# Optimization experiments

Measured on AMD Instinct MI355X. Metric: run time of the kernel, lower is better.

The kernel has to match this reference:

```python
import jax, jax.numpy as jnp
import numpy as np

EPS = 1e-6
N_NODES = 50000
N_EDGES = 800000
IN_DIM = 128
OUT_DIM = 128
HEADS = 4
D_K = OUT_DIM // HEADS
ATT_DIM = 2 * D_K + 1  # use_edge_feat=True


def setup_inputs() -> dict:
    key = jax.random.key(0)
    ks = jax.random.split(key, 8)
    h = jax.random.normal(ks[0], (N_NODES, IN_DIM), dtype=jnp.float32)
    edge_index = jax.random.randint(ks[1], (2, N_EDGES), 0, N_NODES, dtype=jnp.int64)
    edge_feat = jax.random.normal(ks[2], (N_EDGES, 1), dtype=jnp.float32)
    # parameters
    W_w = jax.random.normal(ks[3], (OUT_DIM, IN_DIM), dtype=jnp.float32) / np.sqrt(IN_DIM)
    W_b = jnp.zeros((OUT_DIM,), dtype=jnp.float32)
    att = jax.random.normal(ks[4], (HEADS, ATT_DIM), dtype=jnp.float32)
    ln_g = jnp.ones((OUT_DIM,), dtype=jnp.float32)
    ln_b = jnp.zeros((OUT_DIM,), dtype=jnp.float32)
    return {"h": h, "edge_index": edge_index, "edge_feat": edge_feat,
            "W_w": W_w, "W_b": W_b, "att": att, "ln_g": ln_g, "ln_b": ln_b}


def _layer_norm(x, g, b):
    mu = jnp.mean(x, axis=-1, keepdims=True)
    var = jnp.mean(jnp.square(x - mu), axis=-1, keepdims=True)
    return (x - mu) * jax.lax.rsqrt(var + 1e-5) * g + b


def reference(h, edge_index, edge_feat, W_w, W_b, att, ln_g, ln_b):
    num_nodes = h.shape[0]
    z = h @ W_w.T + W_b                      # [N, out_dim]
    zr = z.reshape(num_nodes, HEADS, D_K)    # [N, H, d_k]
    src, dst = edge_index[0], edge_index[1]
    h_s = zr[src]                            # [E, H, d_k]
    h_d = zr[dst]                            # [E, H, d_k]
    f_e = jnp.broadcast_to(edge_feat[:, None, :], (edge_feat.shape[0], HEADS, 1))
    concat = jnp.concatenate([h_s, h_d, f_e], axis=-1)  # [E, H, att_dim]
    scores = jnp.sum(concat * att[None], axis=-1)        # [E, H]
    scores = jnp.where(scores >= 0, scores, 0.2 * scores)  # LeakyReLU(0.2)
    scores = jnp.clip(scores, -20.0, 20.0)
    alpha = jnp.exp(scores)                               # [E, H]
    denom = jax.ops.segment_sum(alpha, dst, num_segments=num_nodes)  # [N, H]
    norm_alpha = alpha / (denom[dst] + EPS)               # [E, H]
    weighted = h_s * norm_alpha[..., None]                # [E, H, d_k]
    out = jax.ops.segment_sum(weighted, dst, num_segments=num_nodes)  # [N, H, d_k]
    out = out.reshape(num_nodes, OUT_DIM) + z
    out = _layer_norm(out, ln_g, ln_b)
    return jax.nn.elu(out)
```

## Files before the change

### kernel.cpp

```cpp
#include <hip/hip_runtime.h>
#include <hip/hip_bf16.h>
#include <math.h>

typedef __attribute__((ext_vector_type(8))) short bf16x8;
typedef __attribute__((ext_vector_type(4))) float f32x4;

__device__ __forceinline__ unsigned short f2bf(float f) {
    unsigned u = __float_as_uint(f);
    unsigned r = ((u >> 16) & 1u) + 0x7fffu;
    return (unsigned short)((u + r) >> 16);
}
__device__ __forceinline__ float bfL(unsigned u) { return __uint_as_float(u << 16); }
__device__ __forceinline__ float bfH(unsigned u) { return __uint_as_float(u & 0xffff0000u); }

#define SCORE_NPB 128

__global__ __launch_bounds__(256) void k_prep(const float* __restrict__ W,
                                              const float* __restrict__ bias,
                                              const float* __restrict__ att,
                                              const float* __restrict__ h,
                                              unsigned short* __restrict__ Wb16,
                                              float* __restrict__ s_src,
                                              float* __restrict__ s_dst,
                                              int* __restrict__ head4,
                                              int N, int scoreBlocks) {
    const int t = threadIdx.x;
    const int bid = blockIdx.x;
    if (bid == 0) {
#pragma unroll
        for (int q = 0; q < 8; ++q) {
            int gi = q * 256 + t;
            int kg = gi >> 7, row = gi & 127;
            int kbase = (kg >> 2) * 32 + (kg & 3) * 4;
            unsigned pk[4];
#pragma unroll
            for (int p = 0; p < 4; ++p) {
                int e0 = 2 * p, e1 = 2 * p + 1;
                float v0 = W[(size_t)row * 128 + kbase + (e0 >> 2) * 16 + (e0 & 3)];
                float v1 = W[(size_t)row * 128 + kbase + (e1 >> 2) * 16 + (e1 & 3)];
                pk[p] = ((unsigned)f2bf(v1) << 16) | f2bf(v0);
            }
            *reinterpret_cast<uint4*>(&Wb16[(size_t)gi * 8]) =
                make_uint4(pk[0], pk[1], pk[2], pk[3]);
        }
    } else if (bid <= scoreBlocks) {
        __shared__ float wsdL[2][4][128];
        __shared__ float cs[8];
#pragma unroll
        for (int q = 0; q < 4; ++q) {
            int idx = q * 256 + t;
            int isD = idx >> 9, rem = idx & 511;
            int hd = rem >> 7, k = rem & 127;
            float w = 0.f;
            for (int j = 0; j < 32; ++j)
                w += W[(size_t)(hd * 32 + j) * 128 + k] * att[hd * 65 + isD * 32 + j];
            wsdL[isD][hd][k] = w;
        }
        if (t < 8) {
            int chd = t & 3, cIsD = t >> 2;
            float c = 0.f;
            for (int j = 0; j < 32; ++j)
                c += bias[chd * 32 + j] * att[chd * 65 + cIsD * 32 + j];
            cs[t] = c;
        }
        __syncthreads();
        const int p = t & 7;
#pragma unroll
        for (int it = 0; it < 4; ++it) {
            int node = (bid - 1) * SCORE_NPB + it * 32 + (t >> 3);
            if (node >= N) continue;
            const float* hp = h + (size_t)node * 128 + p * 16;
            float ss[4] = {0.f, 0.f, 0.f, 0.f}, sd[4] = {0.f, 0.f, 0.f, 0.f};
#pragma unroll
            for (int q = 0; q < 4; ++q) {
                float4 hv = *reinterpret_cast<const float4*>(hp + q * 4);
#pragma unroll
                for (int hd = 0; hd < 4; ++hd) {
                    const float* wa = &wsdL[0][hd][p * 16 + q * 4];
                    const float* wb = &wsdL[1][hd][p * 16 + q * 4];
                    ss[hd] += hv.x * wa[0] + hv.y * wa[1] + hv.z * wa[2] + hv.w * wa[3];
                    sd[hd] += hv.x * wb[0] + hv.y * wb[1] + hv.z * wb[2] + hv.w * wb[3];
                }
            }
#pragma unroll
            for (int off = 1; off < 8; off <<= 1)
#pragma unroll
                for (int hd = 0; hd < 4; ++hd) {
                    ss[hd] += __shfl_xor(ss[hd], off);
                    sd[hd] += __shfl_xor(sd[hd], off);
                }
            if (p == 0) {
                *reinterpret_cast<float4*>(&s_src[(size_t)node * 4]) =
                    make_float4(ss[0] + cs[0], ss[1] + cs[1], ss[2] + cs[2], ss[3] + cs[3]);
                *reinterpret_cast<float4*>(&s_dst[(size_t)node * 4]) =
                    make_float4(sd[0] + cs[4], sd[1] + cs[5], sd[2] + cs[6], sd[3] + cs[7]);
            }
        }
    } else {
        int i = ((bid - 1 - scoreBlocks) * 256 + t) * 4;
        if (i < N * 4)
            *reinterpret_cast<int4*>(&head4[i]) = make_int4(-1, -1, -1, -1);
    }
}

__global__ __launch_bounds__(256) void k_work(
        const float* __restrict__ h, const unsigned short* __restrict__ Wb16,
        const float* __restrict__ bias, unsigned short* __restrict__ zb16,
        const int* __restrict__ src, const int* __restrict__ dst,
        const float* __restrict__ ef, const float* __restrict__ att,
        const float* __restrict__ s_src, const float* __restrict__ s_dst,
        int* __restrict__ head4, int4* __restrict__ epkt,
        int N, int E, int gemmBlocks) {
    __shared__ short hS[16 * 64 * 8];
    const int t = threadIdx.x;
    const int bid = blockIdx.x;

    if (bid >= gemmBlocks) {
        int e = (bid - gemmBlocks) * 256 + t;
        if (e >= E) return;
        int s = src[e], d = dst[e];
        float fv = ef[e];
        int prev = atomicExch(&head4[(size_t)d * 4 + (e & 3)], e);
        float4 ss = *reinterpret_cast<const float4*>(&s_src[(size_t)s * 4]);
        float4 sd = *reinterpret_cast<const float4*>(&s_dst[(size_t)d * 4]);
        float aE0 = att[64], aE1 = att[129], aE2 = att[194], aE3 = att[259];
        float sc0 = ss.x + sd.x + fv * aE0;
        float sc1 = ss.y + sd.y + fv * aE1;
        float sc2 = ss.z + sd.z + fv * aE2;
        float sc3 = ss.w + sd.w + fv * aE3;
        sc0 = sc0 >= 0.f ? sc0 : 0.2f * sc0;  sc1 = sc1 >= 0.f ? sc1 : 0.2f * sc1;
        sc2 = sc2 >= 0.f ? sc2 : 0.2f * sc2;  sc3 = sc3 >= 0.f ? sc3 : 0.2f * sc3;
        float a0 = expf(fminf(fmaxf(sc0, -20.f), 20.f));
        float a1 = expf(fminf(fmaxf(sc1, -20.f), 20.f));
        float a2 = expf(fminf(fmaxf(sc2, -20.f), 20.f));
        float a3 = expf(fminf(fmaxf(sc3, -20.f), 20.f));
        epkt[e] = make_int4(s, prev,
            (int)(((unsigned)f2bf(a1) << 16) | f2bf(a0)),
            (int)(((unsigned)f2bf(a3) << 16) | f2bf(a2)));
        return;
    }

    const int by = bid & 1;
    const int n0 = (bid >> 1) * 64;
    const int obase = by * 64;
#pragma unroll
    for (int q = 0; q < 8; ++q) {
        int f = q * 256 + t;
        int nd = f >> 5;
        int k4 = (f & 31) * 4;
        int ks = k4 >> 5, rr = k4 & 31;
        int half = rr >> 4, g = (rr & 15) >> 2;
        int kg = ks * 4 + g;
        int slot = kg * 64 + (nd ^ (kg & 7));
        int hn = n0 + nd; if (hn > N - 1) hn = N - 1;
        float4 v = *reinterpret_cast<const float4*>(&h[(size_t)hn * 128 + k4]);
        uint2 pk = make_uint2(((unsigned)f2bf(v.y) << 16) | f2bf(v.x),
                              ((unsigned)f2bf(v.w) << 16) | f2bf(v.z));
        *reinterpret_cast<uint2*>(&hS[slot * 8 + half * 4]) = pk;
    }
    __syncthreads();

    const int wv = t >> 6, l = t & 63;
    const int la = l & 15, lb = l >> 4;
    const int nbase = wv * 16;
    const int node = n0 + nbase + la;

    bf16x8 hfr[4];
#pragma unroll
    for (int ks = 0; ks < 4; ++ks) {
        int kg = ks * 4 + lb;
        int slot = kg * 64 + ((nbase + la) ^ (kg & 7));
        hfr[ks] = *reinterpret_cast<const bf16x8*>(&hS[slot * 8]);
    }

#pragma unroll
    for (int ot = 0; ot < 4; ++ot) {
        f32x4 acc = {0.f, 0.f, 0.f, 0.f};
#pragma unroll
        for (int ks = 0; ks < 4; ++ks) {
            int kg = ks * 4 + lb;
            bf16x8 wfr = *reinterpret_cast<const bf16x8*>(
                &Wb16[((size_t)kg * 128 + obase + ot * 16 + la) * 8]);
            acc = __builtin_amdgcn_mfma_f32_16x16x32_bf16(wfr, hfr[ks], acc, 0, 0, 0);
        }
        int colb = obase + ot * 16 + lb * 4;
        float4 bq = *reinterpret_cast<const float4*>(&bias[colb]);
        if (node < N) {
            uint2 pk = make_uint2(
                ((unsigned)f2bf(acc[1] + bq.y) << 16) | f2bf(acc[0] + bq.x),
                ((unsigned)f2bf(acc[3] + bq.w) << 16) | f2bf(acc[2] + bq.z));
            *reinterpret_cast<uint2*>(&zb16[(size_t)node * 128 + colb]) = pk;
        }
    }
}

__global__ __launch_bounds__(128) void k_agg_final(const int* __restrict__ head4,
                                                   const int4* __restrict__ epkt,
                                                   const uint4* __restrict__ zb4,
                                                   const float* __restrict__ g,
                                                   const float* __restrict__ bparm,
                                                   float* __restrict__ out, int N) {
    int wave = threadIdx.x >> 6, lane = threadIdx.x & 63;
    int l8 = lane & 7;
    int n = blockIdx.x * 16 + wave * 8 + (lane >> 3);
    if (n >= N) return;
    const int hd = l8 >> 1;
    int4 eh = *reinterpret_cast<const int4*>(&head4[(size_t)n * 4]);
    int e0 = eh.x, e1 = eh.y, e2 = eh.z, e3 = eh.w;
    float X0 = 0.f, X1 = 0.f, X2 = 0.f, X3 = 0.f;
    float X4 = 0.f, X5 = 0.f, X6 = 0.f, X7 = 0.f;
    float X8 = 0.f, X9 = 0.f, Xa = 0.f, Xb = 0.f;
    float Xc = 0.f, Xd = 0.f, Xe = 0.f, Xf = 0.f;
    float da = 0.f;
#define UNPK(P, AV) { unsigned u = (hd & 2) ? (unsigned)(P).w : (unsigned)(P).z; \
    AV = (hd & 1) ? bfH(u) : bfL(u); }
#define STEP(EV) if (EV != -1) { \
        int4 p = epkt[EV]; \
        uint4 q0 = zb4[(size_t)p.x * 16 + l8 * 2]; \
        uint4 q1 = zb4[(size_t)p.x * 16 + l8 * 2 + 1]; \
        float a; UNPK(p, a) \
        X0 += bfL(q0.x) * a; X1 += bfH(q0.x) * a; \
        X2 += bfL(q0.y) * a; X3 += bfH(q0.y) * a; \
        X4 += bfL(q0.z) * a; X5 += bfH(q0.z) * a; \
        X6 += bfL(q0.w) * a; X7 += bfH(q0.w) * a; \
        X8 += bfL(q1.x) * a; X9 += bfH(q1.x) * a; \
        Xa += bfL(q1.y) * a; Xb += bfH(q1.y) * a; \
        Xc += bfL(q1.z) * a; Xd += bfH(q1.z) * a; \
        Xe += bfL(q1.w) * a; Xf += bfH(q1.w) * a; \
        da += a; EV = p.y; }
    while (((e0 & e1) & (e2 & e3)) != -1) {
        STEP(e0) STEP(e1) STEP(e2) STEP(e3)
    }
#undef STEP
#undef UNPK

    float inv = 1.f / (da + 1e-6f);
    uint4 qz0 = zb4[(size_t)n * 16 + l8 * 2];
    uint4 qz1 = zb4[(size_t)n * 16 + l8 * 2 + 1];
    float x0 = X0 * inv + bfL(qz0.x), x1 = X1 * inv + bfH(qz0.x);
    float x2 = X2 * inv + bfL(qz0.y), x3 = X3 * inv + bfH(qz0.y);
    float x4 = X4 * inv + bfL(qz0.z), x5 = X5 * inv + bfH(qz0.z);
    float x6 = X6 * inv + bfL(qz0.w), x7 = X7 * inv + bfH(qz0.w);
    float x8 = X8 * inv + bfL(qz1.x), x9 = X9 * inv + bfH(qz1.x);
    float xa = Xa * inv + bfL(qz1.y), xb = Xb * inv + bfH(qz1.y);
    float xc = Xc * inv + bfL(qz1.z), xd = Xd * inv + bfH(qz1.z);
    float xe = Xe * inv + bfL(qz1.w), xf = Xf * inv + bfH(qz1.w);
    float s = (((x0 + x1) + (x2 + x3)) + ((x4 + x5) + (x6 + x7)))
            + (((x8 + x9) + (xa + xb)) + ((xc + xd) + (xe + xf)));
#pragma unroll
    for (int off = 1; off < 8; off <<= 1) s += __shfl_xor(s, off);
    float mu = s * (1.f / 128.f);
    float d0 = x0 - mu, d1 = x1 - mu, d2 = x2 - mu, d3 = x3 - mu;
    float d4 = x4 - mu, d5 = x5 - mu, d6 = x6 - mu, d7 = x7 - mu;
    float d8 = x8 - mu, d9 = x9 - mu, dA = xa - mu, dB = xb - mu;
    float dC = xc - mu, dD = xd - mu, dE = xe - mu, dF = xf - mu;
    float q = (((d0 * d0 + d1 * d1) + (d2 * d2 + d3 * d3))
             + ((d4 * d4 + d5 * d5) + (d6 * d6 + d7 * d7)))
            + (((d8 * d8 + d9 * d9) + (dA * dA + dB * dB))
             + ((dC * dC + dD * dD) + (dE * dE + dF * dF)));
#pragma unroll
    for (int off = 1; off < 8; off <<= 1) q += __shfl_xor(q, off);
    float rstd = rsqrtf(q * (1.f / 128.f) + 1e-5f);
    const int c = l8 * 16;
    float dv[16] = {d0, d1, d2, d3, d4, d5, d6, d7, d8, d9, dA, dB, dC, dD, dE, dF};
#pragma unroll
    for (int qb = 0; qb < 4; ++qb) {
        float4 gg = *reinterpret_cast<const float4*>(&g[c + qb * 4]);
        float4 bb = *reinterpret_cast<const float4*>(&bparm[c + qb * 4]);
        float y0 = dv[qb * 4 + 0] * rstd * gg.x + bb.x;
        float y1 = dv[qb * 4 + 1] * rstd * gg.y + bb.y;
        float y2 = dv[qb * 4 + 2] * rstd * gg.z + bb.z;
        float y3 = dv[qb * 4 + 3] * rstd * gg.w + bb.w;
        y0 = y0 > 0.f ? y0 : expf(y0) - 1.f;
        y1 = y1 > 0.f ? y1 : expf(y1) - 1.f;
        y2 = y2 > 0.f ? y2 : expf(y2) - 1.f;
        y3 = y3 > 0.f ? y3 : expf(y3) - 1.f;
        *reinterpret_cast<float4*>(&out[(size_t)n * 128 + c + qb * 4]) =
            make_float4(y0, y1, y2, y3);
    }
}

extern "C" void kernel_launch(void* const* d_in, const int* in_sizes, int n_in,
                              void* d_out, int out_size, void* d_ws, size_t ws_size,
                              hipStream_t stream) {
    const float* h   = (const float*)d_in[0];
    const int*   ei  = (const int*)d_in[1];
    const float* ef  = (const float*)d_in[2];
    const float* Ww  = (const float*)d_in[3];
    const float* Wb  = (const float*)d_in[4];
    const float* att = (const float*)d_in[5];
    const float* lng = (const float*)d_in[6];
    const float* lnb = (const float*)d_in[7];
    float* out = (float*)d_out;

    const int N = in_sizes[0] / 128;
    const int E = in_sizes[1] / 2;
    const int* src = ei;
    const int* dst = ei + E;

    char* ws = (char*)d_ws;
    unsigned short* zb16   = (unsigned short*)ws; ws += (size_t)N * 128 * 2;
    unsigned short* Wb16   = (unsigned short*)ws; ws += (size_t)128 * 128 * 2;
    float*          s_src  = (float*)ws;          ws += (size_t)N * 4 * 4;
    float*          s_dst  = (float*)ws;          ws += (size_t)N * 4 * 4;
    int*            head4  = (int*)ws;            ws += (size_t)N * 4 * 4;
    int4*           epkt   = (int4*)ws;           ws += (size_t)E * 16;

    const int scoreBlocks = (N + SCORE_NPB - 1) / SCORE_NPB;
    const int headBlocks  = (N + 255) / 256;
    k_prep<<<1 + scoreBlocks + headBlocks, 256, 0, stream>>>(
        Ww, Wb, att, h, Wb16, s_src, s_dst, head4, N, scoreBlocks);

    const int gemmBlocks = ((N + 63) / 64) * 2;
    const int edgeBlocks = (E + 255) / 256;
    k_work<<<gemmBlocks + edgeBlocks, 256, 0, stream>>>(
        h, Wb16, Wb, zb16, src, dst, ef, att, s_src, s_dst, head4, epkt,
        N, E, gemmBlocks);
    k_agg_final<<<(N + 15) / 16, 128, 0, stream>>>(head4, epkt,
                                                   (const uint4*)zb16, lng, lnb, out, N);
}
```

Baseline: 110.2 us.

## Sort nodes by in-degree bins before aggregation to balance wave work

Counts the in-degree of every node with atomics, builds a 64-bin degree histogram, scans it and produces a node order grouped by degree. The aggregation kernel then processes nodes in that order, so the 8 nodes sharing a wave have similar edge-list lengths and lanes diverge less. It adds three small kernel launches, a counting pass of atomics over all edges, and an indirection through the order array, which scatters the output and z row accesses.

```diff
diff --git a/kernel.cpp b/kernel.cpp
--- a/kernel.cpp
+++ b/kernel.cpp
@@ -23,10 +23,13 @@
                                               float* __restrict__ s_src,
                                               float* __restrict__ s_dst,
                                               int* __restrict__ head4,
-                                              int N, int scoreBlocks) {
+                                              int* __restrict__ counts,
+                                              int* __restrict__ binCnt,
+                                              int N, int scoreBlocks, int headBlocks) {
     const int t = threadIdx.x;
     const int bid = blockIdx.x;
     if (bid == 0) {
+        if (t < 64) binCnt[t] = 0;
 #pragma unroll
         for (int q = 0; q < 8; ++q) {
             int gi = q * 256 + t;
@@ -96,10 +99,14 @@
                     make_float4(sd[0] + cs[4], sd[1] + cs[5], sd[2] + cs[6], sd[3] + cs[7]);
             }
         }
-    } else {
+    } else if (bid <= scoreBlocks + headBlocks) {
         int i = ((bid - 1 - scoreBlocks) * 256 + t) * 4;
         if (i < N * 4)
             *reinterpret_cast<int4*>(&head4[i]) = make_int4(-1, -1, -1, -1);
+    } else {
+        int i = ((bid - 1 - scoreBlocks - headBlocks) * 256 + t) * 4;
+        if (i < N)
+            *reinterpret_cast<int4*>(&counts[i]) = make_int4(0, 0, 0, 0);
     }
 }
 
@@ -110,11 +117,21 @@
         const float* __restrict__ ef, const float* __restrict__ att,
         const float* __restrict__ s_src, const float* __restrict__ s_dst,
         int* __restrict__ head4, int4* __restrict__ epkt,
-        int N, int E, int gemmBlocks) {
+        int* __restrict__ counts,
+        int N, int E, int gemmBlocks, int edgeBlocks) {
     __shared__ short hS[16 * 64 * 8];
     const int t = threadIdx.x;
     const int bid = blockIdx.x;
 
+    if (bid >= gemmBlocks + edgeBlocks) {
+        int base = (bid - gemmBlocks - edgeBlocks) * 1024 + t;
+#pragma unroll
+        for (int q = 0; q < 4; ++q) {
+            int e = base + q * 256;
+            if (e < E) atomicAdd(&counts[dst[e]], 1);
+        }
+        return;
+    }
     if (bid >= gemmBlocks) {
         int e = (bid - gemmBlocks) * 256 + t;
         if (e >= E) return;
@@ -194,7 +211,52 @@
     }
 }
 
-__global__ __launch_bounds__(128) void k_agg_final(const int* __restrict__ head4,
+__global__ __launch_bounds__(256) void k_binhist(const int* __restrict__ counts,
+                                                 int* __restrict__ binCnt, int N) {
+    __shared__ int lh[64];
+    int t = threadIdx.x;
+    if (t < 64) lh[t] = 0;
+    __syncthreads();
+    int i = blockIdx.x * 256 + t;
+    if (i < N) atomicAdd(&lh[min(counts[i], 63)], 1);
+    __syncthreads();
+    if (t < 64 && lh[t] > 0) atomicAdd(&binCnt[t], lh[t]);
+}
+
+__global__ void k_binscan(const int* __restrict__ binCnt,
+                          int* __restrict__ binCur) {
+    int lane = threadIdx.x & 63;
+    int x = binCnt[lane];
+    int own = x;
+#pragma unroll
+    for (int d = 1; d < 64; d <<= 1) {
+        int v = __shfl_up(x, d);
+        if (lane >= d) x += v;
+    }
+    binCur[lane] = x - own;
+}
+
+__global__ __launch_bounds__(256) void k_order(const int* __restrict__ counts,
+                                               int* __restrict__ binCur,
+                                               int* __restrict__ order, int N) {
+    __shared__ int lh[64], base[64];
+    int t = threadIdx.x;
+    if (t < 64) lh[t] = 0;
+    __syncthreads();
+    int i = blockIdx.x * 256 + t;
+    int b = 0, lrank = 0;
+    if (i < N) {
+        b = min(counts[i], 63);
+        lrank = atomicAdd(&lh[b], 1);
+    }
+    __syncthreads();
+    if (t < 64 && lh[t] > 0) base[t] = atomicAdd(&binCur[t], lh[t]);
+    __syncthreads();
+    if (i < N) order[base[b] + lrank] = i;
+}
+
+__global__ __launch_bounds__(128) void k_agg_final(const int* __restrict__ order,
+                                                   const int* __restrict__ head4,
                                                    const int4* __restrict__ epkt,
                                                    const uint4* __restrict__ zb4,
                                                    const float* __restrict__ g,
@@ -202,8 +264,9 @@
                                                    float* __restrict__ out, int N) {
     int wave = threadIdx.x >> 6, lane = threadIdx.x & 63;
     int l8 = lane & 7;
-    int n = blockIdx.x * 16 + wave * 8 + (lane >> 3);
-    if (n >= N) return;
+    int slot = blockIdx.x * 16 + wave * 8 + (lane >> 3);
+    if (slot >= N) return;
+    const int n = order[slot];
     const int hd = l8 >> 1;
     int4 eh = *reinterpret_cast<const int4*>(&head4[(size_t)n * 4]);
     int e0 = eh.x, e1 = eh.y, e2 = eh.z, e3 = eh.w;
@@ -304,18 +367,31 @@
     float*          s_src  = (float*)ws;          ws += (size_t)N * 4 * 4;
     float*          s_dst  = (float*)ws;          ws += (size_t)N * 4 * 4;
     int*            head4  = (int*)ws;            ws += (size_t)N * 4 * 4;
+    int*            counts = (int*)ws;            ws += (size_t)N * 4;
+    int*            order  = (int*)ws;            ws += (size_t)N * 4;
+    int*            binCnt = (int*)ws;            ws += (size_t)64 * 4;
+    int*            binCur = (int*)ws;            ws += (size_t)64 * 4;
     int4*           epkt   = (int4*)ws;           ws += (size_t)E * 16;
 
     const int scoreBlocks = (N + SCORE_NPB - 1) / SCORE_NPB;
     const int headBlocks  = (N + 255) / 256;
-    k_prep<<<1 + scoreBlocks + headBlocks, 256, 0, stream>>>(
-        Ww, Wb, att, h, Wb16, s_src, s_dst, head4, N, scoreBlocks);
+    const int cntBlocks   = (N / 4 + 255) / 256;
+    k_prep<<<1 + scoreBlocks + headBlocks + cntBlocks, 256, 0, stream>>>(
+        Ww, Wb, att, h, Wb16, s_src, s_dst, head4, counts, binCnt,
+        N, scoreBlocks, headBlocks);
 
     const int gemmBlocks = ((N + 63) / 64) * 2;
     const int edgeBlocks = (E + 255) / 256;
-    k_work<<<gemmBlocks + edgeBlocks, 256, 0, stream>>>(
-        h, Wb16, Wb, zb16, src, dst, ef, att, s_src, s_dst, head4, epkt,
-        N, E, gemmBlocks);
-    k_agg_final<<<(N + 15) / 16, 128, 0, stream>>>(head4, epkt,
+    const int histBlocks = (E + 1023) / 1024;
+    k_work<<<gemmBlocks + edgeBlocks + histBlocks, 256, 0, stream>>>(
+        h, Wb16, Wb, zb16, src, dst, ef, att, s_src, s_dst, head4, epkt, counts,
+        N, E, gemmBlocks, edgeBlocks);
+
+    const int nodeBlocks = (N + 255) / 256;
+    k_binhist<<<nodeBlocks, 256, 0, stream>>>(counts, binCnt, N);
+    k_binscan<<<1, 64, 0, stream>>>(binCnt, binCur);
+    k_order<<<nodeBlocks, 256, 0, stream>>>(counts, binCur, order, N);
+
+    k_agg_final<<<(N + 15) / 16, 128, 0, stream>>>(order, head4, epkt,
                                                    (const uint4*)zb16, lng, lnb, out, N);
 }
```

Measured after the change: 158.1 us. 1.43x slower.
